# Kernel tuning notes

Measured on AMD Instinct MI355X. Metric: run time of the kernel, lower is better.

## Reference

```python
import jax, jax.numpy as jnp
import numpy as np

EPS = 1e-5
H, W, C, NCLS = 8, 16, 64, 8

def _bn_params(key, c):
    k1, k2, k3, k4 = jax.random.split(key, 4)
    gamma = jax.random.uniform(k1, (c,), minval=0.5, maxval=1.5)
    beta = 0.1 * jax.random.normal(k2, (c,))
    mean = 0.1 * jax.random.normal(k3, (c,))
    var = jax.random.uniform(k4, (c,), minval=0.5, maxval=1.5)
    return jnp.stack([gamma, beta, mean, var]).astype(jnp.float32)  # (4, c)

def bn2d(x, p):
    # eval-mode BatchNorm2d; p: (4, C); x: (B, C, H, W)
    g, b, m, v = p[0], p[1], p[2], p[3]
    s = g * jax.lax.rsqrt(v + EPS)
    return x * s[None, :, None, None] + (b - m * s)[None, :, None, None]

def bn1d_scalar(x, p):
    # eval-mode BatchNorm1d with 1 channel; p: (4, 1); x: (B, 1, F)
    g, b, m, v = p[0], p[1], p[2], p[3]
    s = g * jax.lax.rsqrt(v + EPS)
    return x * s + (b - m * s)

def conv_same(x, w, b):
    y = jax.lax.conv_general_dilated(x, w, (1, 1), 'SAME',
                                     dimension_numbers=('NCHW', 'OIHW', 'NCHW'))
    return y + b[None, :, None, None]

def setup_inputs() -> dict:
    key = jax.random.key(0)
    ks = jax.random.split(key, 24)
    B = 8192
    d = {}
    d['x'] = jax.random.normal(ks[0], (B, 1, H, W), dtype=jnp.float32)
    d['bn0'] = _bn_params(ks[1], 1)
    d['conv1_w'] = 0.1 * jax.random.normal(ks[2], (C, 1, 3, 3), dtype=jnp.float32)
    d['conv1_b'] = jnp.zeros((C,), jnp.float32)
    d['bn1'] = _bn_params(ks[3], C)
    d['conv2_w'] = (0.1 / np.sqrt(C)) * jax.random.normal(ks[4], (C, C, 3, 3), dtype=jnp.float32)
    d['conv2_b'] = jnp.zeros((C,), jnp.float32)
    d['bn2'] = _bn_params(ks[5], C)
    # LocallyConnected2d, kernel_size=1 -> per-pixel (out_c, in_c) weights
    d['lc3_w'] = (1.0 / np.sqrt(C)) * jax.random.normal(ks[6], (C, C, H, W), dtype=jnp.float32)
    d['bn3'] = _bn_params(ks[7], C)
    d['lc4_w'] = (1.0 / np.sqrt(C)) * jax.random.normal(ks[8], (C, C, H, W), dtype=jnp.float32)
    d['bn4'] = _bn_params(ks[9], C)
    F5 = H * W * C
    d['fc5_w'] = (1.0 / np.sqrt(F5)) * jax.random.normal(ks[10], (512, F5), dtype=jnp.float32)
    d['fc5_b'] = jnp.zeros((512,), jnp.float32)
    d['bn5'] = _bn_params(ks[11], 1)
    d['fc6_w'] = (1.0 / np.sqrt(512)) * jax.random.normal(ks[12], (512, 512), dtype=jnp.float32)
    d['fc6_b'] = jnp.zeros((512,), jnp.float32)
    d['bn6'] = _bn_params(ks[13], 1)
    d['fc7_w'] = (1.0 / np.sqrt(512)) * jax.random.normal(ks[14], (128, 512), dtype=jnp.float32)
    d['fc7_b'] = jnp.zeros((128,), jnp.float32)
    d['bn7'] = _bn_params(ks[15], 1)
    d['fc8_w'] = (1.0 / np.sqrt(128)) * jax.random.normal(ks[16], (NCLS, 128), dtype=jnp.float32)
    d['fc8_b'] = jnp.zeros((NCLS,), jnp.float32)
    return d

def reference(x, bn0, conv1_w, conv1_b, bn1, conv2_w, conv2_b, bn2,
              lc3_w, bn3, lc4_w, bn4, fc5_w, fc5_b, bn5,
              fc6_w, fc6_b, bn6, fc7_w, fc7_b, bn7, fc8_w, fc8_b):
    B = x.shape[0]
    # squeeze -> view(B, 16, 8) -> transpose(1,2) -> add channel dim
    h = jnp.swapaxes(x.reshape(B, W, H), 1, 2)[:, None]  # (B,1,H,W)
    h = bn2d(h, bn0)
    h = jax.nn.relu(bn2d(conv_same(h, conv1_w, conv1_b), bn1))
    h = jax.nn.relu(bn2d(conv_same(h, conv2_w, conv2_b), bn2))
    # locally connected, k=1: per-pixel channel mixing
    h = jax.nn.relu(bn2d(jnp.einsum('bchw,ochw->bohw', h, lc3_w), bn3))
    h = jax.nn.relu(bn2d(jnp.einsum('bchw,ochw->bohw', h, lc4_w), bn4))
    h = h.reshape(B, 1, -1)  # (B, 1, C*H*W)
    h = h @ fc5_w.T + fc5_b
    h = jax.nn.relu(bn1d_scalar(h, bn5))
    h = jax.nn.relu(bn1d_scalar(h @ fc6_w.T + fc6_b, bn6))
    h = jax.nn.relu(bn1d_scalar(h @ fc7_w.T + fc7_b, bn7))
    h = h @ fc8_w.T + fc8_b
    return h.reshape(B, NCLS)
```

## Files before the change

kernel.cpp:

```cpp
#include <hip/hip_runtime.h>
#include <hip/hip_bf16.h>

typedef unsigned short bf16_t;
typedef __attribute__((ext_vector_type(8))) short bf16x8;
typedef __attribute__((ext_vector_type(8))) unsigned short u16x8;
typedef __attribute__((ext_vector_type(4))) float f32x4;

#if defined(__has_builtin)
#if __has_builtin(__builtin_amdgcn_global_load_lds)
#define HAS_GLL 1
#endif
#endif

__device__ __forceinline__ float b2f(bf16_t u) {
    return __uint_as_float(((unsigned int)u) << 16);
}
__device__ __forceinline__ bf16_t f2b(float f) {
    unsigned int x = __float_as_uint(f);
    unsigned int r = x + 0x7fffu + ((x >> 16) & 1u);
    return (bf16_t)(r >> 16);
}
__device__ __forceinline__ unsigned int pk2(float a, float b) {
    __hip_bfloat162 t = __float22bfloat162_rn(make_float2(a, b));
    return *(unsigned int*)&t;
}
__device__ __forceinline__ float ldf(const void* p, int i, int isf) {
    return isf ? ((const float*)p)[i] : b2f(((const bf16_t*)p)[i]);
}
__device__ __forceinline__ u16x8 ld8(const void* p, size_t off, int isf) {
    u16x8 o;
    if (isf) {
        const float* f = (const float*)p + off;
        #pragma unroll
        for (int j = 0; j < 8; j++) o[j] = f2b(f[j]);
    } else {
        o = *(const u16x8*)((const bf16_t*)p + off);
    }
    return o;
}

__device__ __forceinline__ void stg16(const bf16_t* g, bf16_t* l) {
#ifdef HAS_GLL
    __builtin_amdgcn_global_load_lds(
        (const __attribute__((address_space(1))) unsigned int*)g,
        (__attribute__((address_space(3))) unsigned int*)l,
        16, 0, 0);
#else
    *(uint4*)l = *(const uint4*)g;
#endif
}

__device__ __forceinline__ int detect_isf(const void* xraw) {
    const unsigned int* w = (const unsigned int*)xraw;
    unsigned int u = w[threadIdx.x & 63];
    float a = fabsf(__uint_as_float(u << 16));
    int g = (a >= 0.0009765625f && a <= 16.0f) ? 1 : 0;
    unsigned long long m = __ballot(g);
    return (__builtin_popcountll(m) >= 32) ? 0 : 1;
}

#define OFF_S0T0 0
#define OFF_W1   16
#define OFF_S1   592
#define OFF_H1   656
#define OFF_S2   720
#define OFF_H2   784
#define OFF_S3   848
#define OFF_H3   912
#define OFF_S4   976
#define OFF_H4   1040
#define OFF_SC5  1104
#define OFF_H5   1112
#define OFF_SC6  1624
#define OFF_H6   1632
#define OFF_SC7  2144
#define OFF_H7   2152
#define OFF_W8   2280
#define OFF_B8   3304
#define OFF_FLAG 4032

__global__ __launch_bounds__(256) void setup_fold_kernel(
    const void* __restrict__ x,
    const void* __restrict__ w2, const void* __restrict__ w3,
    const void* __restrict__ w4, const void* __restrict__ w5,
    const void* __restrict__ w6, const void* __restrict__ w7,
    bf16_t* __restrict__ w2p, bf16_t* __restrict__ w3p,
    bf16_t* __restrict__ w4p, bf16_t* __restrict__ w5p,
    bf16_t* __restrict__ w6b, bf16_t* __restrict__ w7b,
    const void* __restrict__ bn0p, const void* __restrict__ w1,
    const void* __restrict__ b1, const void* __restrict__ bn1p,
    const void* __restrict__ b2c, const void* __restrict__ bn2p,
    const void* __restrict__ bn3p, const void* __restrict__ bn4p,
    const void* __restrict__ b5, const void* __restrict__ bn5p,
    const void* __restrict__ b6, const void* __restrict__ bn6p,
    const void* __restrict__ b7, const void* __restrict__ bn7p,
    const void* __restrict__ w8, const void* __restrict__ b8,
    float* __restrict__ prm)
{
    const int t  = threadIdx.x;
    const int bb = blockIdx.x;
    const int isf = detect_isf(x);

    if (bb < 512) {
        __shared__ unsigned short ls[128 * 66];
        const int nr = bb;
        const size_t so = (size_t)nr * 8192;
        #pragma unroll
        for (int k = 0; k < 4; k++) {
            const int e0 = (t + k * 256) * 8;
            u16x8 v = ld8(w5, so + e0, isf);
            const int c = e0 >> 7, p0 = e0 & 127;
            #pragma unroll
            for (int j = 0; j < 8; j++) ls[(p0 + j) * 66 + c] = v[j];
        }
        __syncthreads();
        #pragma unroll
        for (int k = 0; k < 4; k++) {
            const int d0 = (t + k * 256) * 8;
            const int p = d0 >> 6, c0 = d0 & 63;
            u16x8 o;
            #pragma unroll
            for (int j = 0; j < 8; j++) o[j] = ls[p * 66 + c0 + j];
            *(u16x8*)(w5p + so + d0) = o;
        }
        return;
    }
    if (bb < 640) {
        __shared__ unsigned short ls[128 * 66];
        const int oc = (bb - 512) & 63;
        const void* src = (bb < 576) ? w3 : w4;
        bf16_t*    dst = (bb < 576) ? w3p : w4p;
        const size_t so = (size_t)oc * 8192;
        #pragma unroll
        for (int k = 0; k < 4; k++) {
            const int e0 = (t + k * 256) * 8;
            u16x8 v = ld8(src, so + e0, isf);
            const int ic = e0 >> 7, p0 = e0 & 127;
            #pragma unroll
            for (int j = 0; j < 8; j++) ls[(p0 + j) * 66 + ic] = v[j];
        }
        __syncthreads();
        #pragma unroll
        for (int k = 0; k < 4; k++) {
            const int d0 = (t + k * 256) * 8;
            const int p = d0 >> 6, ic0 = d0 & 63;
            u16x8 o;
            #pragma unroll
            for (int j = 0; j < 8; j++) o[j] = ls[p * 66 + ic0 + j];
            *(u16x8*)(dst + (size_t)p * 4096 + oc * 64 + ic0) = o;
        }
        return;
    }
    if (bb < 768) {
        const int i0 = ((bb - 640) * 256 + t) * 8;
        *(u16x8*)(w6b + i0) = ld8(w6, i0, isf);
        return;
    }
    if (bb < 800) {
        const int i0 = ((bb - 768) * 256 + t) * 8;
        *(u16x8*)(w7b + i0) = ld8(w7, i0, isf);
        return;
    }
    if (bb < 944) {
        const int i = (bb - 800) * 256 + t;
        int oc = i / 576, r = i - oc * 576;
        int tap = r >> 6, ic = r & 63;
        w2p[i] = f2b(ldf(w2, oc * 576 + ic * 9 + tap, isf));
        return;
    }

    if (t == 0) prm[OFF_FLAG] = isf ? 1.0f : 0.0f;

    if (t == 0) {
        float g = ldf(bn0p, 0, isf), be = ldf(bn0p, 1, isf);
        float m = ldf(bn0p, 2, isf), v = ldf(bn0p, 3, isf);
        float s = g * rsqrtf(v + 1e-5f);
        prm[OFF_S0T0] = s; prm[OFF_S0T0 + 1] = be - m * s;
    }
    for (int i = t; i < 576; i += 256) prm[OFF_W1 + i] = ldf(w1, i, isf);

    if (t < 64) {
        {
            float g = ldf(bn1p, t, isf), be = ldf(bn1p, 64 + t, isf);
            float m = ldf(bn1p, 128 + t, isf), v = ldf(bn1p, 192 + t, isf);
            float s = g * rsqrtf(v + 1e-5f);
            prm[OFF_S1 + t] = s;
            prm[OFF_H1 + t] = s * ldf(b1, t, isf) + (be - m * s);
        }
        {
            float g = ldf(bn2p, t, isf), be = ldf(bn2p, 64 + t, isf);
            float m = ldf(bn2p, 128 + t, isf), v = ldf(bn2p, 192 + t, isf);
            float s = g * rsqrtf(v + 1e-5f);
            prm[OFF_S2 + t] = s;
            prm[OFF_H2 + t] = s * ldf(b2c, t, isf) + (be - m * s);
        }
        {
            float g = ldf(bn3p, t, isf), be = ldf(bn3p, 64 + t, isf);
            float m = ldf(bn3p, 128 + t, isf), v = ldf(bn3p, 192 + t, isf);
            float s = g * rsqrtf(v + 1e-5f);
            prm[OFF_S3 + t] = s;
            prm[OFF_H3 + t] = be - m * s;
        }
        {
            float g = ldf(bn4p, t, isf), be = ldf(bn4p, 64 + t, isf);
            float m = ldf(bn4p, 128 + t, isf), v = ldf(bn4p, 192 + t, isf);
            float s = g * rsqrtf(v + 1e-5f);
            prm[OFF_S4 + t] = s;
            prm[OFF_H4 + t] = be - m * s;
        }
    }
    {
        float g = ldf(bn5p, 0, isf), be = ldf(bn5p, 1, isf);
        float m = ldf(bn5p, 2, isf), v = ldf(bn5p, 3, isf);
        float s = g * rsqrtf(v + 1e-5f);
        if (t == 0) prm[OFF_SC5] = s;
        for (int i = t; i < 512; i += 256)
            prm[OFF_H5 + i] = s * ldf(b5, i, isf) + (be - m * s);
    }
    {
        float g = ldf(bn6p, 0, isf), be = ldf(bn6p, 1, isf);
        float m = ldf(bn6p, 2, isf), v = ldf(bn6p, 3, isf);
        float s = g * rsqrtf(v + 1e-5f);
        if (t == 0) prm[OFF_SC6] = s;
        for (int i = t; i < 512; i += 256)
            prm[OFF_H6 + i] = s * ldf(b6, i, isf) + (be - m * s);
    }
    {
        float g = ldf(bn7p, 0, isf), be = ldf(bn7p, 1, isf);
        float m = ldf(bn7p, 2, isf), v = ldf(bn7p, 3, isf);
        float s = g * rsqrtf(v + 1e-5f);
        if (t == 0) prm[OFF_SC7] = s;
        if (t < 128) prm[OFF_H7 + t] = s * ldf(b7, t, isf) + (be - m * s);
    }
    for (int i = t; i < 1024; i += 256) prm[OFF_W8 + i] = ldf(w8, i, isf);
    if (t < 8) prm[OFF_B8 + t] = ldf(b8, t, isf);
}

__global__ __launch_bounds__(256) void conv1_kernel(
    const void* __restrict__ x, const float* __restrict__ prm,
    bf16_t* __restrict__ c1, int Bc, int c0)
{
    __shared__ float xn[720];
    __shared__ float w1s[576];

    const int t = threadIdx.x;
    const int b0 = blockIdx.x * 4;
    const int isf = prm[OFF_FLAG] > 0.5f;
    const float s0 = prm[OFF_S0T0], t0 = prm[OFF_S0T0 + 1];

    for (int i = t; i < 576; i += 256) w1s[i] = prm[OFF_W1 + i];
    for (int i = t; i < 720; i += 256) {
        int s = i / 180, r = i - s * 180;
        int row = r / 18, col = r - row * 18;
        float v = 0.f;
        if (row >= 1 && row <= 8 && col >= 1 && col <= 16)
            v = s0 * ldf(x, (c0 + b0 + s) * 128 + (col - 1) * 8 + (row - 1), isf) + t0;
        xn[i] = v;
    }

    const int oc0 = (t & 7) * 8;
    const int pg  = t >> 3;

    float s1[8], h1[8];
    #pragma unroll
    for (int j = 0; j < 8; j++) {
        s1[j] = prm[OFF_S1 + oc0 + j];
        h1[j] = prm[OFF_H1 + oc0 + j];
    }
    __syncthreads();

    for (int s = 0; s < 4; s++) {
        const int b = b0 + s;
        const float* xs = xn + s * 180;
        #pragma unroll
        for (int m = 0; m < 4; m++) {
            int p = pg + 32 * m;
            int h = p >> 4, w = p & 15;
            float r[9];
            #pragma unroll
            for (int dh = 0; dh < 3; dh++)
                #pragma unroll
                for (int dw = 0; dw < 3; dw++)
                    r[dh * 3 + dw] = xs[(h + dh) * 18 + (w + dw)];
            u16x8 o;
            #pragma unroll
            for (int j = 0; j < 8; j++) {
                float acc = 0.f;
                #pragma unroll
                for (int k = 0; k < 9; k++) acc += r[k] * w1s[(oc0 + j) * 9 + k];
                o[j] = f2b(fmaxf(s1[j] * acc + h1[j], 0.f));
            }
            *(u16x8*)(c1 + (size_t)p * Bc * 64 + (size_t)b * 64 + oc0) = o;
        }
    }
}

__global__ __launch_bounds__(256) void fused_mfma_kernel(
    const bf16_t* __restrict__ c1, const bf16_t* __restrict__ w2p,
    const bf16_t* __restrict__ w3p, const bf16_t* __restrict__ w4p,
    const float* __restrict__ prm, bf16_t* __restrict__ bufA, int Bc)
{
    __shared__ bf16_t sm[20480];
    const int t    = threadIdx.x;
    const int lane = t & 63;
    const int wv   = t >> 6;

    int btile, p;
    {
        const int nbx = gridDim.x;
        const int id = blockIdx.x + nbx * blockIdx.y;
        if ((nbx & 7) == 0) {
            const int xcd = id & 7;
            const int k   = id >> 3;
            p     = k & 127;
            btile = xcd + 8 * (k >> 7);
        } else {
            btile = blockIdx.x; p = blockIdx.y;
        }
    }
    const int m0 = btile * 256;
    const int h  = p >> 4, w = p & 15;

    const int fr = lane & 15;
    const int fg = lane >> 4;
    const int swz4 = (fr >> 1) & 3;

    const int gS    = (t & 3) ^ ((t >> 3) & 3);
    const int rA    = t >> 2;
    const int coff0 = rA * 64 + gS * 8;
    const int w2off = rA * 576 + gS * 8;

    u16x8 wr3[2], wr4[2];
    {
        const bf16_t* w3b = w3p + (size_t)p * 4096 + coff0;
        const bf16_t* w4b = w4p + (size_t)p * 4096 + coff0;
        wr3[0] = *(const u16x8*)(w3b);
        wr3[1] = *(const u16x8*)(w3b + 32);
        wr4[0] = *(const u16x8*)(w4b);
        wr4[1] = *(const u16x8*)(w4b + 32);
    }

    f32x4 acc[4][4];
    #pragma unroll
    for (int i = 0; i < 4; i++)
        #pragma unroll
        for (int j = 0; j < 4; j++)
            acc[i][j] = (f32x4){0.f, 0.f, 0.f, 0.f};

    const bf16_t* c1b = c1 + (size_t)m0 * 64 + coff0;
    const size_t planeStride = (size_t)Bc * 64;

    {
        if (h > 0 && w > 0) {
            const bf16_t* ab = c1b + (size_t)((h - 1) * 16 + (w - 1)) * planeStride;
            #pragma unroll
            for (int u = 0; u < 4; u++)
                stg16(ab + u * 4096, sm + t * 8 + u * 2048);
            stg16(w2p + w2off, sm + 16384 + t * 8);
        }
    }
    #pragma unroll
    for (int s = 0; s < 18; s++) {
        const int cur = s & 1;
        __syncthreads();
        if (s + 1 < 18) {
            const int s1  = s + 1;
            const int tap = s1 >> 1;
            const int dh = tap / 3 - 1, dw = tap % 3 - 1;
            const int hh = h + dh, ww = w + dw;
            if (hh >= 0 && hh < 8 && ww >= 0 && ww < 16) {
                const int nb  = cur ^ 1;
                const int ic0 = (s1 & 1) * 32;
                const bf16_t* ab = c1b + (size_t)(hh * 16 + ww) * planeStride + ic0;
                #pragma unroll
                for (int u = 0; u < 4; u++)
                    stg16(ab + u * 4096, sm + nb * 8192 + t * 8 + u * 2048);
                stg16(w2p + w2off + tap * 64 + ic0, sm + 16384 + nb * 2048 + t * 8);
            }
        }
        {
            const int tap = s >> 1;
            const int dh = tap / 3 - 1, dw = tap % 3 - 1;
            const int hh = h + dh, ww = w + dw;
            if (hh >= 0 && hh < 8 && ww >= 0 && ww < 16) {
                const bf16_t* Ab = sm + cur * 8192;
                const bf16_t* Bb = sm + 16384 + cur * 2048;
                bf16x8 hf[4], wf[4];
                #pragma unroll
                for (int j = 0; j < 4; j++)
                    hf[j] = *(const bf16x8*)(Ab + ((wv * 64 + j * 16 + fr) * 4 + (fg ^ swz4)) * 8);
                #pragma unroll
                for (int i = 0; i < 4; i++)
                    wf[i] = *(const bf16x8*)(Bb + ((i * 16 + fr) * 4 + (fg ^ swz4)) * 8);
                #pragma unroll
                for (int i = 0; i < 4; i++)
                    #pragma unroll
                    for (int j = 0; j < 4; j++)
                        acc[i][j] = __builtin_amdgcn_mfma_f32_16x16x32_bf16(
                            wf[i], hf[j], acc[i][j], 0, 0, 0);
            }
        }
    }
    __syncthreads();

#define EPILOGUE(SOFF, HOFF)                                                  \
    _Pragma("unroll")                                                         \
    for (int i = 0; i < 4; i++) {                                             \
        const int oc0e = i * 16 + fg * 4;                                     \
        const float4 sv = *(const float4*)(prm + (SOFF) + oc0e);              \
        const float4 hv = *(const float4*)(prm + (HOFF) + oc0e);              \
        _Pragma("unroll")                                                     \
        for (int j = 0; j < 4; j++) {                                         \
            const int bi = wv * 64 + j * 16 + fr;                             \
            float v0 = fmaxf(sv.x * acc[i][j][0] + hv.x, 0.f);                \
            float v1 = fmaxf(sv.y * acc[i][j][1] + hv.y, 0.f);                \
            float v2 = fmaxf(sv.z * acc[i][j][2] + hv.z, 0.f);                \
            float v3 = fmaxf(sv.w * acc[i][j][3] + hv.w, 0.f);                \
            uint2 pk; pk.x = pk2(v0, v1); pk.y = pk2(v2, v3);                 \
            *(uint2*)(sm + bi * 72 + oc0e) = pk;                              \
        }                                                                     \
    }

    EPILOGUE(OFF_S2, OFF_H2)
    *(u16x8*)(sm + 18432 + t * 8) = wr3[0];
    __syncthreads();

    #pragma unroll
    for (int i = 0; i < 4; i++)
        #pragma unroll
        for (int j = 0; j < 4; j++)
            acc[i][j] = (f32x4){0.f, 0.f, 0.f, 0.f};

    #pragma unroll
    for (int ks = 0; ks < 2; ks++) {
        if (ks == 1) {
            __syncthreads();
            *(u16x8*)(sm + 18432 + t * 8) = wr3[1];
            __syncthreads();
        }
        bf16x8 hf[4], wf[4];
        #pragma unroll
        for (int j = 0; j < 4; j++)
            hf[j] = *(const bf16x8*)(sm + (wv * 64 + j * 16 + fr) * 72 + ks * 32 + fg * 8);
        #pragma unroll
        for (int i = 0; i < 4; i++)
            wf[i] = *(const bf16x8*)(sm + 18432 + ((i * 16 + fr) * 4 + (fg ^ swz4)) * 8);
        #pragma unroll
        for (int i = 0; i < 4; i++)
            #pragma unroll
            for (int j = 0; j < 4; j++)
                acc[i][j] = __builtin_amdgcn_mfma_f32_16x16x32_bf16(
                    wf[i], hf[j], acc[i][j], 0, 0, 0);
    }

    EPILOGUE(OFF_S3, OFF_H3)
    __syncthreads();
    *(u16x8*)(sm + 18432 + t * 8) = wr4[0];
    __syncthreads();

    #pragma unroll
    for (int i = 0; i < 4; i++)
        #pragma unroll
        for (int j = 0; j < 4; j++)
            acc[i][j] = (f32x4){0.f, 0.f, 0.f, 0.f};

    #pragma unroll
    for (int ks = 0; ks < 2; ks++) {
        if (ks == 1) {
            __syncthreads();
            *(u16x8*)(sm + 18432 + t * 8) = wr4[1];
            __syncthreads();
        }
        bf16x8 hf[4], wf[4];
        #pragma unroll
        for (int j = 0; j < 4; j++)
            hf[j] = *(const bf16x8*)(sm + (wv * 64 + j * 16 + fr) * 72 + ks * 32 + fg * 8);
        #pragma unroll
        for (int i = 0; i < 4; i++)
            wf[i] = *(const bf16x8*)(sm + 18432 + ((i * 16 + fr) * 4 + (fg ^ swz4)) * 8);
        #pragma unroll
        for (int i = 0; i < 4; i++)
            #pragma unroll
            for (int j = 0; j < 4; j++)
                acc[i][j] = __builtin_amdgcn_mfma_f32_16x16x32_bf16(
                    wf[i], hf[j], acc[i][j], 0, 0, 0);
    }

    EPILOGUE(OFF_S4, OFF_H4)
#undef EPILOGUE
    __syncthreads();

    const int orow = t >> 3, wc0 = (t & 7) * 8;
    #pragma unroll
    for (int pass = 0; pass < 8; pass++) {
        const int row = orow + pass * 32;
        *(uint4*)(bufA + (size_t)(m0 + row) * 8192 + p * 64 + wc0) =
            *(const uint4*)(sm + row * 72 + wc0);
    }
}

__global__ __launch_bounds__(256) void gemm_mfma(
    const bf16_t* __restrict__ A, const bf16_t* __restrict__ W,
    const float* __restrict__ prm, int sc_off, int sh_off,
    bf16_t* __restrict__ out, int K, int N)
{
    __shared__ bf16_t sm[24576];
    const int t    = threadIdx.x;
    const int lane = t & 63;
    const int wv   = t >> 6;
    const int wr   = wv >> 1, wc = wv & 1;

    int bm, bn;
    {
        const int nx = gridDim.x, ny = gridDim.y;
        const int id = blockIdx.x + nx * blockIdx.y;
        if ((nx & 7) == 0) {
            const int xcd = id & 7;
            const int k   = id >> 3;
            const int pl  = k / ny;
            bn = k - pl * ny;
            bm = xcd + 8 * pl;
        } else {
            bm = blockIdx.x; bn = blockIdx.y;
        }
    }
    const int m0 = bm * 128, n0 = bn * 64;

    const int fr = lane & 15;
    const int fg = lane >> 4;
    const int swz8 = fr & 7;

    const bf16_t* srcA[4]; bf16_t* dstA[4];
    #pragma unroll
    for (int u = 0; u < 4; u++) {
        const int c = t + 256 * u;
        const int row = c >> 3;
        const int g = (c & 7) ^ (row & 7);
        srcA[u] = A + (size_t)(m0 + row) * K + g * 8;
        dstA[u] = sm + c * 8;
    }
    const bf16_t* srcB[2]; bf16_t* dstB[2];
    #pragma unroll
    for (int u = 0; u < 2; u++) {
        const int c = t + 256 * u;
        const int row = c >> 3;
        const int g = (c & 7) ^ (row & 7);
        srcB[u] = W + (size_t)(n0 + row) * K + g * 8;
        dstB[u] = sm + 16384 + c * 8;
    }

    f32x4 acc[4][2];
    #pragma unroll
    for (int i = 0; i < 4; i++)
        #pragma unroll
        for (int j = 0; j < 2; j++)
            acc[i][j] = (f32x4){0.f, 0.f, 0.f, 0.f};

    const int KS = K >> 6;

    #pragma unroll
    for (int u = 0; u < 4; u++) stg16(srcA[u], dstA[u]);
    #pragma unroll
    for (int u = 0; u < 2; u++) stg16(srcB[u], dstB[u]);

    for (int ks = 0; ks < KS; ks++) {
        const int cur = ks & 1;
        __syncthreads();
        if (ks + 1 < KS) {
            const int nb = cur ^ 1;
            const int kk = (ks + 1) << 6;
            #pragma unroll
            for (int u = 0; u < 4; u++) stg16(srcA[u] + kk, dstA[u] + nb * 8192);
            #pragma unroll
            for (int u = 0; u < 2; u++) stg16(srcB[u] + kk, dstB[u] + nb * 4096);
        }
        const bf16_t* Ab = sm + cur * 8192;
        const bf16_t* Bb = sm + 16384 + cur * 4096;
        bf16x8 af[4][2], bf2[2][2];
        #pragma unroll
        for (int i = 0; i < 4; i++)
            #pragma unroll
            for (int hh = 0; hh < 2; hh++) {
                const int r = wr * 64 + i * 16 + fr;
                const int g = hh * 4 + fg;
                af[i][hh] = *(const bf16x8*)(Ab + (r * 8 + (g ^ swz8)) * 8);
            }
        #pragma unroll
        for (int j = 0; j < 2; j++)
            #pragma unroll
            for (int hh = 0; hh < 2; hh++) {
                const int r = wc * 32 + j * 16 + fr;
                const int g = hh * 4 + fg;
                bf2[j][hh] = *(const bf16x8*)(Bb + (r * 8 + (g ^ swz8)) * 8);
            }
        #pragma unroll
        for (int hh = 0; hh < 2; hh++)
            #pragma unroll
            for (int i = 0; i < 4; i++)
                #pragma unroll
                for (int j = 0; j < 2; j++)
                    acc[i][j] = __builtin_amdgcn_mfma_f32_16x16x32_bf16(
                        af[i][hh], bf2[j][hh], acc[i][j], 0, 0, 0);
    }

    const float s    = prm[sc_off];
    const int   orow = fg * 4;
    const int   ocol = fr;
    #pragma unroll
    for (int j = 0; j < 2; j++) {
        const int n  = n0 + wc * 32 + j * 16 + ocol;
        const float sh = prm[sh_off + n];
        #pragma unroll
        for (int i = 0; i < 4; i++) {
            const int mb = m0 + wr * 64 + i * 16 + orow;
            #pragma unroll
            for (int r = 0; r < 4; r++) {
                float v = fmaxf(s * acc[i][j][r] + sh, 0.f);
                out[(size_t)(mb + r) * N + n] = f2b(v);
            }
        }
    }
}

__global__ __launch_bounds__(256) void fc8_kernel(
    const bf16_t* __restrict__ h, const float* __restrict__ prm,
    void* __restrict__ out, int c0)
{
    __shared__ float wsm[8 * 129];
    const int t = threadIdx.x;
    for (int i = t; i < 1024; i += 256) {
        int n = i >> 7, k = i & 127;
        wsm[n * 129 + k] = prm[OFF_W8 + i];
    }
    __syncthreads();
    const int isf = prm[OFF_FLAG] > 0.5f;
    const int bl = t >> 3, n = t & 7;
    const int b = c0 + blockIdx.x * 32 + bl;
    const bf16_t* hb = h + (size_t)(blockIdx.x * 32 + bl) * 128;
    float acc = prm[OFF_B8 + n];
    #pragma unroll
    for (int k8 = 0; k8 < 16; k8++) {
        u16x8 hv = *(const u16x8*)(hb + k8 * 8);
        #pragma unroll
        for (int j = 0; j < 8; j++)
            acc += b2f(hv[j]) * wsm[n * 129 + k8 * 8 + j];
    }
    if (isf) ((float*)out)[(size_t)b * 8 + n] = acc;
    else     ((bf16_t*)out)[(size_t)b * 8 + n] = f2b(acc);
}

extern "C" void kernel_launch(void* const* d_in, const int* in_sizes, int n_in,
                              void* d_out, int out_size, void* d_ws, size_t ws_size,
                              hipStream_t stream)
{
    const void* x    = d_in[0];
    const void* bn0p = d_in[1];
    const void* w1   = d_in[2];
    const void* b1   = d_in[3];
    const void* bn1p = d_in[4];
    const void* w2   = d_in[5];
    const void* b2c  = d_in[6];
    const void* bn2p = d_in[7];
    const void* w3   = d_in[8];
    const void* bn3p = d_in[9];
    const void* w4   = d_in[10];
    const void* bn4p = d_in[11];
    const void* w5   = d_in[12];
    const void* b5   = d_in[13];
    const void* bn5p = d_in[14];
    const void* w6   = d_in[15];
    const void* b6   = d_in[16];
    const void* bn6p = d_in[17];
    const void* w7   = d_in[18];
    const void* b7   = d_in[19];
    const void* bn7p = d_in[20];
    const void* w8   = d_in[21];
    const void* b8   = d_in[22];

    char* base = (char*)d_ws;
    float*  prm = (float*)(base + 0);
    bf16_t* w2p = (bf16_t*)(base + 16384);
    bf16_t* w3p = (bf16_t*)(base + 90112);
    bf16_t* w4p = (bf16_t*)(base + 1138688);
    bf16_t* w5p = (bf16_t*)(base + 2187264);
    bf16_t* w6b = (bf16_t*)(base + 10575872);
    bf16_t* w7b = (bf16_t*)(base + 11100160);
    char*   acts = base + 11231232;

    const int B = 8192;
    const size_t FIXED = 11231232ull;

    setup_fold_kernel<<<945, 256, 0, stream>>>(
        x, w2, w3, w4, w5, w6, w7, w2p, w3p, w4p, w5p, w6b, w7b,
        bn0p, w1, b1, bn1p, b2c, bn2p, bn3p, bn4p,
        b5, bn5p, b6, bn6p, b7, bn7p, w8, b8, prm);

    const size_t NEED_1PASS = FIXED + (size_t)B * 16384ull + (size_t)B * 18688ull;
    const size_t NEED_2PASS = FIXED + 4096ull * 16384ull + (size_t)B * 18688ull;

    if (ws_size >= NEED_2PASS) {
        const int Bf = (ws_size >= NEED_1PASS) ? 8192 : 4096;

        bf16_t* c1   = (bf16_t*)acts;
        bf16_t* bufA = c1 + (size_t)Bf * 8192;
        bf16_t* bufC = bufA + (size_t)B * 8192;
        bf16_t* bufD = bufC + (size_t)B * 512;
        bf16_t* bufE = bufD + (size_t)B * 512;

        for (int c0 = 0; c0 < B; c0 += Bf) {
            conv1_kernel<<<Bf / 4, 256, 0, stream>>>(x, prm, c1, Bf, c0);
            fused_mfma_kernel<<<dim3(Bf / 256, 128), 256, 0, stream>>>(
                c1, w2p, w3p, w4p, prm, bufA + (size_t)c0 * 8192, Bf);
        }
        gemm_mfma<<<dim3(B / 128, 8), 256, 0, stream>>>(
            bufA, w5p, prm, OFF_SC5, OFF_H5, bufC, 8192, 512);
        gemm_mfma<<<dim3(B / 128, 8), 256, 0, stream>>>(
            bufC, w6b, prm, OFF_SC6, OFF_H6, bufD, 512, 512);
        gemm_mfma<<<dim3(B / 128, 2), 256, 0, stream>>>(
            bufD, w7b, prm, OFF_SC7, OFF_H7, bufE, 512, 128);
        fc8_kernel<<<B / 32, 256, 0, stream>>>(bufE, prm, d_out, 0);
    } else {
        size_t avail = (ws_size > FIXED) ? (ws_size - FIXED) : 0;
        int Bc = 8192;
        while (Bc > 256 && (size_t)Bc * 35072ull > avail) Bc >>= 1;

        bf16_t* c1   = (bf16_t*)acts;
        bf16_t* bufA = c1 + (size_t)Bc * 8192;
        bf16_t* bufC = bufA + (size_t)Bc * 8192;
        bf16_t* bufD = bufC + (size_t)Bc * 512;
        bf16_t* bufE = bufD + (size_t)Bc * 512;

        for (int c0 = 0; c0 < B; c0 += Bc) {
            conv1_kernel<<<Bc / 4, 256, 0, stream>>>(x, prm, c1, Bc, c0);
            fused_mfma_kernel<<<dim3(Bc / 256, 128), 256, 0, stream>>>(
                c1, w2p, w3p, w4p, prm, bufA, Bc);
            gemm_mfma<<<dim3(Bc / 128, 8), 256, 0, stream>>>(
                bufA, w5p, prm, OFF_SC5, OFF_H5, bufC, 8192, 512);
            gemm_mfma<<<dim3(Bc / 128, 8), 256, 0, stream>>>(
                bufC, w6b, prm, OFF_SC6, OFF_H6, bufD, 512, 512);
            gemm_mfma<<<dim3(Bc / 128, 2), 256, 0, stream>>>(
                bufD, w7b, prm, OFF_SC7, OFF_H7, bufE, 512, 128);
            fc8_kernel<<<Bc / 32, 256, 0, stream>>>(bufE, prm, d_out, c0);
        }
    }
}
```

Before: 401.6 us.

## Fuse conv1 into setup kernel and merge fc7 with fc8

Adds extra blocks to the setup/fold kernel that compute conv1+BN1+ReLU directly, so the separate conv1 launch is skipped when the whole batch fits in one pass. Replaces the fc7 GEMM and the fc8 kernel with one fc78 kernel that runs the 512->128 MFMA GEMM, keeps the activated tile in LDS and applies the 128->8 projection in place. This removes two kernel launches and an intermediate global round trip, at the cost of a larger LDS footprint per block and conv1 blocks sharing a launch with the weight-folding blocks.

```diff
diff --git a/kernel.cpp b/kernel.cpp
--- a/kernel.cpp
+++ b/kernel.cpp
@@ -95,11 +95,73 @@
     const void* __restrict__ b6, const void* __restrict__ bn6p,
     const void* __restrict__ b7, const void* __restrict__ bn7p,
     const void* __restrict__ w8, const void* __restrict__ b8,
-    float* __restrict__ prm)
+    float* __restrict__ prm, bf16_t* __restrict__ c1, int Bf)
 {
     const int t  = threadIdx.x;
     const int bb = blockIdx.x;
     const int isf = detect_isf(x);
+
+    if (bb >= 945) {
+        const int b0 = (bb - 945) * 4;
+        __shared__ float xn[720];
+        __shared__ float w1s[576];
+
+        float s0, t0;
+        {
+            float g = ldf(bn0p, 0, isf), be = ldf(bn0p, 1, isf);
+            float m = ldf(bn0p, 2, isf), v = ldf(bn0p, 3, isf);
+            s0 = g * rsqrtf(v + 1e-5f); t0 = be - m * s0;
+        }
+        for (int i = t; i < 576; i += 256) w1s[i] = ldf(w1, i, isf);
+        for (int i = t; i < 720; i += 256) {
+            int s = i / 180, r = i - s * 180;
+            int row = r / 18, col = r - row * 18;
+            float v = 0.f;
+            if (row >= 1 && row <= 8 && col >= 1 && col <= 16)
+                v = s0 * ldf(x, (b0 + s) * 128 + (col - 1) * 8 + (row - 1), isf) + t0;
+            xn[i] = v;
+        }
+
+        const int oc0 = (t & 7) * 8;
+        const int pg  = t >> 3;
+
+        float s1[8], h1[8];
+        #pragma unroll
+        for (int j = 0; j < 8; j++) {
+            const int ch = oc0 + j;
+            float g = ldf(bn1p, ch, isf), be = ldf(bn1p, 64 + ch, isf);
+            float m = ldf(bn1p, 128 + ch, isf), v = ldf(bn1p, 192 + ch, isf);
+            s1[j] = g * rsqrtf(v + 1e-5f);
+            h1[j] = s1[j] * ldf(b1, ch, isf) + (be - m * s1[j]);
+        }
+        __syncthreads();
+
+        for (int s = 0; s < 4; s++) {
+            const int b = b0 + s;
+            const float* xs = xn + s * 180;
+            #pragma unroll
+            for (int m = 0; m < 4; m++) {
+                int p = pg + 32 * m;
+                int h = p >> 4, w = p & 15;
+                float r[9];
+                #pragma unroll
+                for (int dh = 0; dh < 3; dh++)
+                    #pragma unroll
+                    for (int dw = 0; dw < 3; dw++)
+                        r[dh * 3 + dw] = xs[(h + dh) * 18 + (w + dw)];
+                u16x8 o;
+                #pragma unroll
+                for (int j = 0; j < 8; j++) {
+                    float acc = 0.f;
+                    #pragma unroll
+                    for (int k = 0; k < 9; k++) acc += r[k] * w1s[(oc0 + j) * 9 + k];
+                    o[j] = f2b(fmaxf(s1[j] * acc + h1[j], 0.f));
+                }
+                *(u16x8*)(c1 + (size_t)p * Bf * 64 + (size_t)b * 64 + oc0) = o;
+            }
+        }
+        return;
+    }
 
     if (bb < 512) {
         __shared__ unsigned short ls[128 * 66];
@@ -622,31 +684,135 @@
     }
 }
 
-__global__ __launch_bounds__(256) void fc8_kernel(
-    const bf16_t* __restrict__ h, const float* __restrict__ prm,
-    void* __restrict__ out, int c0)
+__global__ __launch_bounds__(256) void fc78_kernel(
+    const bf16_t* __restrict__ A, const bf16_t* __restrict__ W,
+    const float* __restrict__ prm, void* __restrict__ out, int c0)
 {
-    __shared__ float wsm[8 * 129];
-    const int t = threadIdx.x;
-    for (int i = t; i < 1024; i += 256) {
-        int n = i >> 7, k = i & 127;
-        wsm[n * 129 + k] = prm[OFF_W8 + i];
-    }
+    __shared__ bf16_t sm[32768];
+    const int t    = threadIdx.x;
+    const int lane = t & 63;
+    const int wv   = t >> 6;
+    const int wr   = wv >> 1, wc = wv & 1;
+    const int m0   = blockIdx.x * 128;
+    const int K    = 512;
+
+    const int fr = lane & 15;
+    const int fg = lane >> 4;
+    const int swz8 = fr & 7;
+
+    const bf16_t* srcA[4]; bf16_t* dstA[4];
+    #pragma unroll
+    for (int u = 0; u < 4; u++) {
+        const int c = t + 256 * u;
+        const int row = c >> 3;
+        const int g = (c & 7) ^ (row & 7);
+        srcA[u] = A + (size_t)(m0 + row) * K + g * 8;
+        dstA[u] = sm + c * 8;
+    }
+    const bf16_t* srcB[4]; bf16_t* dstB[4];
+    #pragma unroll
+    for (int u = 0; u < 4; u++) {
+        const int c = t + 256 * u;
+        const int row = c >> 3;
+        const int g = (c & 7) ^ (row & 7);
+        srcB[u] = W + (size_t)row * K + g * 8;
+        dstB[u] = sm + 16384 + c * 8;
+    }
+
+    f32x4 acc[4][4];
+    #pragma unroll
+    for (int i = 0; i < 4; i++)
+        #pragma unroll
+        for (int j = 0; j < 4; j++)
+            acc[i][j] = (f32x4){0.f, 0.f, 0.f, 0.f};
+
+    const int KS = 8;
+
+    #pragma unroll
+    for (int u = 0; u < 4; u++) stg16(srcA[u], dstA[u]);
+    #pragma unroll
+    for (int u = 0; u < 4; u++) stg16(srcB[u], dstB[u]);
+
+    for (int ks = 0; ks < KS; ks++) {
+        const int cur = ks & 1;
+        __syncthreads();
+        if (ks + 1 < KS) {
+            const int nb = cur ^ 1;
+            const int kk = (ks + 1) << 6;
+            #pragma unroll
+            for (int u = 0; u < 4; u++) stg16(srcA[u] + kk, dstA[u] + nb * 8192);
+            #pragma unroll
+            for (int u = 0; u < 4; u++) stg16(srcB[u] + kk, dstB[u] + nb * 8192);
+        }
+        const bf16_t* Ab = sm + cur * 8192;
+        const bf16_t* Bb = sm + 16384 + cur * 8192;
+        bf16x8 af[4][2], bf2[4][2];
+        #pragma unroll
+        for (int i = 0; i < 4; i++)
+            #pragma unroll
+            for (int hh = 0; hh < 2; hh++) {
+                const int r = wr * 64 + i * 16 + fr;
+                const int g = hh * 4 + fg;
+                af[i][hh] = *(const bf16x8*)(Ab + (r * 8 + (g ^ swz8)) * 8);
+            }
+        #pragma unroll
+        for (int j = 0; j < 4; j++)
+            #pragma unroll
+            for (int hh = 0; hh < 2; hh++) {
+                const int r = wc * 64 + j * 16 + fr;
+                const int g = hh * 4 + fg;
+                bf2[j][hh] = *(const bf16x8*)(Bb + (r * 8 + (g ^ swz8)) * 8);
+            }
+        #pragma unroll
+        for (int hh = 0; hh < 2; hh++)
+            #pragma unroll
+            for (int i = 0; i < 4; i++)
+                #pragma unroll
+                for (int j = 0; j < 4; j++)
+                    acc[i][j] = __builtin_amdgcn_mfma_f32_16x16x32_bf16(
+                        af[i][hh], bf2[j][hh], acc[i][j], 0, 0, 0);
+    }
+
     __syncthreads();
+    float* w8s = (float*)(sm + 16640);
+    for (int i = t; i < 1024; i += 256) w8s[i] = prm[OFF_W8 + i];
+
+    const float s = prm[OFF_SC7];
+    #pragma unroll
+    for (int j = 0; j < 4; j++) {
+        const int n  = wc * 64 + j * 16 + fr;
+        const float sh = prm[OFF_H7 + n];
+        #pragma unroll
+        for (int i = 0; i < 4; i++) {
+            const int row0 = wr * 64 + i * 16 + fg * 4;
+            #pragma unroll
+            for (int r = 0; r < 4; r++) {
+                float v = fmaxf(s * acc[i][j][r] + sh, 0.f);
+                sm[(row0 + r) * 130 + n] = f2b(v);
+            }
+        }
+    }
+    __syncthreads();
+
     const int isf = prm[OFF_FLAG] > 0.5f;
-    const int bl = t >> 3, n = t & 7;
-    const int b = c0 + blockIdx.x * 32 + bl;
-    const bf16_t* hb = h + (size_t)(blockIdx.x * 32 + bl) * 128;
-    float acc = prm[OFF_B8 + n];
-    #pragma unroll
-    for (int k8 = 0; k8 < 16; k8++) {
-        u16x8 hv = *(const u16x8*)(hb + k8 * 8);
-        #pragma unroll
-        for (int j = 0; j < 8; j++)
-            acc += b2f(hv[j]) * wsm[n * 129 + k8 * 8 + j];
-    }
-    if (isf) ((float*)out)[(size_t)b * 8 + n] = acc;
-    else     ((bf16_t*)out)[(size_t)b * 8 + n] = f2b(acc);
+    const int r   = t & 127;
+    const int n4  = (t >> 7) * 4;
+    float a4[4];
+    #pragma unroll
+    for (int q = 0; q < 4; q++) a4[q] = prm[OFF_B8 + n4 + q];
+    for (int k = 0; k < 128; k++) {
+        const float hv = b2f(sm[r * 130 + k]);
+        #pragma unroll
+        for (int q = 0; q < 4; q++) a4[q] += hv * w8s[(n4 + q) * 128 + k];
+    }
+    const size_t ob = (size_t)(c0 + m0 + r) * 8 + n4;
+    if (isf) {
+        float4 o4 = make_float4(a4[0], a4[1], a4[2], a4[3]);
+        *(float4*)((float*)out + ob) = o4;
+    } else {
+        uint2 pk; pk.x = pk2(a4[0], a4[1]); pk.y = pk2(a4[2], a4[3]);
+        *(uint2*)((bf16_t*)out + ob) = pk;
+    }
 }
 
 extern "C" void kernel_launch(void* const* d_in, const int* in_sizes, int n_in,
@@ -690,11 +856,6 @@
     const int B = 8192;
     const size_t FIXED = 11231232ull;
 
-    setup_fold_kernel<<<945, 256, 0, stream>>>(
-        x, w2, w3, w4, w5, w6, w7, w2p, w3p, w4p, w5p, w6b, w7b,
-        bn0p, w1, b1, bn1p, b2c, bn2p, bn3p, bn4p,
-        b5, bn5p, b6, bn6p, b7, bn7p, w8, b8, prm);
-
     const size_t NEED_1PASS = FIXED + (size_t)B * 16384ull + (size_t)B * 18688ull;
     const size_t NEED_2PASS = FIXED + 4096ull * 16384ull + (size_t)B * 18688ull;
 
@@ -705,10 +866,16 @@
         bf16_t* bufA = c1 + (size_t)Bf * 8192;
         bf16_t* bufC = bufA + (size_t)B * 8192;
         bf16_t* bufD = bufC + (size_t)B * 512;
-        bf16_t* bufE = bufD + (size_t)B * 512;
+
+        const int extra = (Bf == 8192) ? Bf / 4 : 0;
+        setup_fold_kernel<<<945 + extra, 256, 0, stream>>>(
+            x, w2, w3, w4, w5, w6, w7, w2p, w3p, w4p, w5p, w6b, w7b,
+            bn0p, w1, b1, bn1p, b2c, bn2p, bn3p, bn4p,
+            b5, bn5p, b6, bn6p, b7, bn7p, w8, b8, prm, c1, Bf);
 
         for (int c0 = 0; c0 < B; c0 += Bf) {
-            conv1_kernel<<<Bf / 4, 256, 0, stream>>>(x, prm, c1, Bf, c0);
+            if (extra == 0)
+                conv1_kernel<<<Bf / 4, 256, 0, stream>>>(x, prm, c1, Bf, c0);
             fused_mfma_kernel<<<dim3(Bf / 256, 128), 256, 0, stream>>>(
                 c1, w2p, w3p, w4p, prm, bufA + (size_t)c0 * 8192, Bf);
         }
@@ -716,9 +883,7 @@
             bufA, w5p, prm, OFF_SC5, OFF_H5, bufC, 8192, 512);
         gemm_mfma<<<dim3(B / 128, 8), 256, 0, stream>>>(
             bufC, w6b, prm, OFF_SC6, OFF_H6, bufD, 512, 512);
-        gemm_mfma<<<dim3(B / 128, 2), 256, 0, stream>>>(
-            bufD, w7b, prm, OFF_SC7, OFF_H7, bufE, 512, 128);
-        fc8_kernel<<<B / 32, 256, 0, stream>>>(bufE, prm, d_out, 0);
+        fc78_kernel<<<B / 128, 256, 0, stream>>>(bufD, w7b, prm, d_out, 0);
     } else {
         size_t avail = (ws_size > FIXED) ? (ws_size - FIXED) : 0;
         int Bc = 8192;
@@ -728,7 +893,11 @@
         bf16_t* bufA = c1 + (size_t)Bc * 8192;
         bf16_t* bufC = bufA + (size_t)Bc * 8192;
         bf16_t* bufD = bufC + (size_t)Bc * 512;
-        bf16_t* bufE = bufD + (size_t)Bc * 512;
+
+        setup_fold_kernel<<<945, 256, 0, stream>>>(
+            x, w2, w3, w4, w5, w6, w7, w2p, w3p, w4p, w5p, w6b, w7b,
+            bn0p, w1, b1, bn1p, b2c, bn2p, bn3p, bn4p,
+            b5, bn5p, b6, bn6p, b7, bn7p, w8, b8, prm, c1, Bc);
 
         for (int c0 = 0; c0 < B; c0 += Bc) {
             conv1_kernel<<<Bc / 4, 256, 0, stream>>>(x, prm, c1, Bc, c0);
@@ -738,9 +907,7 @@
                 bufA, w5p, prm, OFF_SC5, OFF_H5, bufC, 8192, 512);
             gemm_mfma<<<dim3(Bc / 128, 8), 256, 0, stream>>>(
                 bufC, w6b, prm, OFF_SC6, OFF_H6, bufD, 512, 512);
-            gemm_mfma<<<dim3(Bc / 128, 2), 256, 0, stream>>>(
-                bufD, w7b, prm, OFF_SC7, OFF_H7, bufE, 512, 128);
-            fc8_kernel<<<Bc / 32, 256, 0, stream>>>(bufE, prm, d_out, c0);
-        }
-    }
-}
+            fc78_kernel<<<Bc / 128, 256, 0, stream>>>(bufD, w7b, prm, d_out, c0);
+        }
+    }
+}
```

New measurement: 390.1 us, median of 2. 2.9% less time.
